# Performance work log

Hardware: AMD Instinct MI355X
Metric: run time of the kernel (lower is better)

The kernel has to match this reference:

```python
import jax, jax.numpy as jnp
import numpy as np

E = 1024      # embedding_size
K = 64        # key_size
D = 64        # head_size
S = 1024      # context_size
V = 32000     # vocab_size
H = 16        # layer_size (heads per layer)
L = 8         # num_layers
B = 2


def _pe():
    pos = jnp.arange(S, dtype=jnp.float32)[:, None]
    i = jnp.arange(E, dtype=jnp.float32)[None, :]
    ang = pos / jnp.power(10000.0, 2.0 * i / E)
    return jnp.where((jnp.arange(E) % 2 == 0)[None, :], jnp.sin(ang), jnp.cos(ang))


def setup_inputs() -> dict:
    key = jax.random.key(0)
    ks = iter(jax.random.split(key, 32))
    s = 0.02
    n = lambda shape: jax.random.normal(next(ks), shape, dtype=jnp.float32) * s
    inp = {
        "tokens": jax.random.randint(next(ks), (B, S), 0, V),
        "emb": n((V, E)),
        "pe": _pe(),
        "k1w": n((L, H, K, E)), "k1b": n((L, H, K)),
        "k2w": n((L, H, K, K)), "k2b": n((L, H, K)),
        "q1w": n((L, H, K, E)), "q1b": n((L, H, K)),
        "q2w": n((L, H, K, K)), "q2b": n((L, H, K)),
        "vw": n((L, H, D, E)), "vb": n((L, H, D)),
        "lnw": jnp.ones((L, E), jnp.float32), "lnb": jnp.zeros((L, E), jnp.float32),
        "p1w": n((L, E, E)), "p1b": n((L, E)),
        "p2w": n((L, E, E)), "p2b": n((L, E)),
        "predw": n((V, E)), "predb": n((V,)),
    }
    return inp


def reference(tokens, emb, pe, k1w, k1b, k2w, k2b, q1w, q1b, q2w, q2b,
              vw, vb, lnw, lnb, p1w, p1b, p2w, p2b, predw, predb):
    relu = jax.nn.relu
    x = emb[tokens] + pe[:tokens.shape[1]]                       # [B,S,E]
    seq = tokens.shape[1]
    # Faithful to original: tril (past+diag) gets the -1e10 penalty.
    mask = jnp.tril(jnp.ones((seq, seq), x.dtype)) * -1e10
    for l in range(L):
        # two-layer ReLU MLPs for K and Q, batched over heads
        k = relu(jnp.einsum('bse,hke->bhsk', x, k1w[l]) + k1b[l][None, :, None, :])
        k = relu(jnp.einsum('bhsk,hjk->bhsj', k, k2w[l]) + k2b[l][None, :, None, :])
        q = relu(jnp.einsum('bse,hke->bhsk', x, q1w[l]) + q1b[l][None, :, None, :])
        q = relu(jnp.einsum('bhsk,hjk->bhsj', q, q2w[l]) + q2b[l][None, :, None, :])
        v = jnp.einsum('bse,hde->bhsd', x, vw[l]) + vb[l][None, :, None, :]
        scores = jnp.einsum('bhsk,bhtk->bhst', q, k) / (K ** 0.5) + mask
        w = jax.nn.softmax(scores, axis=-1)
        o = jnp.einsum('bhst,bhtd->bhsd', w, v)                  # [B,H,S,D]
        o = o.transpose(0, 2, 1, 3).reshape(x.shape[0], seq, H * D)
        y = x + o
        mu = y.mean(-1, keepdims=True)
        var = ((y - mu) ** 2).mean(-1, keepdims=True)
        yn = (y - mu) / jnp.sqrt(var + 1e-5) * lnw[l] + lnb[l]
        h1 = relu(yn @ p1w[l].T + p1b[l])
        x = relu(h1 @ p2w[l].T + p2b[l])
    logits = x @ predw.T + predb                                 # [B,S,V]
    return logits
```

## Files before the change

### kernel.cpp

```cpp
#include <hip/hip_runtime.h>


typedef __attribute__((ext_vector_type(8))) short bf16x8;
typedef __attribute__((ext_vector_type(4))) float f32x4;

#define L_ 8
#define S_ 1024
#define E_ 1024
#define B_ 2
#define H_ 16
#define V_ 32000
#define M_ 2048

__device__ __forceinline__ unsigned short f2b(float f) {
  union { float f; unsigned int u; } v; v.f = f;
  unsigned int r = v.u + 0x7FFFu + ((v.u >> 16) & 1u);
  return (unsigned short)(r >> 16);
}

#define GLDS16(gptr, lptr)                                                            \
  __builtin_amdgcn_global_load_lds(                                                   \
      (const __attribute__((address_space(1))) unsigned int*)(gptr),                  \
      (__attribute__((address_space(3))) unsigned int*)(lptr), 16, 0, 0)

__global__ void cvt_all_kernel(
    const float* __restrict__ k1w, const float* __restrict__ q1w,
    const float* __restrict__ vw,  const float* __restrict__ k2w,
    const float* __restrict__ q2w, const float* __restrict__ p1w,
    const float* __restrict__ p2w, const float* __restrict__ predw,
    unsigned short* __restrict__ wcat, unsigned short* __restrict__ wk2,
    unsigned short* __restrict__ wq2,  unsigned short* __restrict__ wp1,
    unsigned short* __restrict__ wp2,  unsigned short* __restrict__ wpred) {
  size_t u = (size_t)blockIdx.x * 256 + threadIdx.x;
  const float* src; unsigned short* dst;
  if (u < 6291456) {
    int seg = (int)(u / 2097152);
    size_t e0 = (u - (size_t)seg * 2097152) * 4;
    const float* s = (seg == 0) ? k1w : (seg == 1) ? q1w : vw;
    src = s + e0;
    int l = (int)(e0 >> 20), off = (int)(e0 & 1048575);
    dst = wcat + (size_t)l * 3145728 + (size_t)seg * 1048576 + off;
  } else if (u < 6422528) { size_t e = (u - 6291456) * 4;  src = k2w + e;   dst = wk2 + e; }
  else if (u < 6553600)   { size_t e = (u - 6422528) * 4;  src = q2w + e;   dst = wq2 + e; }
  else if (u < 8650752)   { size_t e = (u - 6553600) * 4;  src = p1w + e;   dst = wp1 + e; }
  else if (u < 10747904)  { size_t e = (u - 8650752) * 4;  src = p2w + e;   dst = wp2 + e; }
  else                    { size_t e = (u - 10747904) * 4; src = predw + e; dst = wpred + e; }
  float4 v = *(const float4*)src;
  dst[0] = f2b(v.x); dst[1] = f2b(v.y); dst[2] = f2b(v.z); dst[3] = f2b(v.w);
}

__global__ void biascat_kernel(const float* __restrict__ k1b, const float* __restrict__ q1b,
                               const float* __restrict__ vb, float* __restrict__ bcat) {
  int i = blockIdx.x * 256 + threadIdx.x;
  int l = i / 3072, j = i - l * 3072;
  float v;
  if (j < 1024)      v = k1b[l * 1024 + j];
  else if (j < 2048) v = q1b[l * 1024 + j - 1024];
  else               v = vb [l * 1024 + j - 2048];
  bcat[i] = v;
}

__global__ void embed_kernel(const int* __restrict__ tokens, const float* __restrict__ emb,
                             const float* __restrict__ pe, float* __restrict__ x32,
                             unsigned short* __restrict__ xb) {
  int row = blockIdx.x;
  int s = row & (S_ - 1);
  int e0 = threadIdx.x * 4;
  int tok = tokens[row];
  float4 ev = *(const float4*)(emb + (size_t)tok * E_ + e0);
  float4 pv = *(const float4*)(pe + (size_t)s * E_ + e0);
  float4 v; v.x = ev.x + pv.x; v.y = ev.y + pv.y; v.z = ev.z + pv.z; v.w = ev.w + pv.w;
  *(float4*)(x32 + (size_t)row * E_ + e0) = v;
  ushort4 o; o.x = f2b(v.x); o.y = f2b(v.y); o.z = f2b(v.z); o.w = f2b(v.w);
  *(ushort4*)(xb + (size_t)row * E_ + e0) = o;
}

template <int BM, int BN, int RELU, int OBF, int OF32, int VT, int K2Q2>
__global__ __launch_bounds__(256) void gemm97(
    const unsigned short* __restrict__ A, const unsigned short* __restrict__ W,
    const float* __restrict__ bias, unsigned short* __restrict__ Cb,
    float* __restrict__ Cf, unsigned short* __restrict__ vTp,
    const unsigned short* __restrict__ wk2p, const unsigned short* __restrict__ wq2p,
    const float* __restrict__ k2bp, const float* __restrict__ q2bp,
    unsigned short* __restrict__ kbufp, unsigned short* __restrict__ qbufp,
    int K, int N, int reluN) {
  constexpr int AR = BM / 64;
  constexpr int BR = BN / 64;
  constexpr int FM = BM / 32;
  constexpr int FN = BN / 32;
  __shared__ __align__(16) unsigned short sA[BM * 32];
  __shared__ __align__(16) unsigned short sB[BN * 32];
  __shared__ __align__(16) unsigned short sC[K2Q2 ? 128 * 136 : 1];
  const int tid = threadIdx.x;
  const int lane = tid & 63, wave = tid >> 6;
  const int l16 = lane & 15, lhi = lane >> 4;

  const int gx = gridDim.x, nwg = gx * gridDim.y;
  int o = blockIdx.y * gx + blockIdx.x;
  int wg = ((nwg & 7) == 0) ? ((o & 7) * (nwg >> 3) + (o >> 3)) : o;
  const int row0 = (wg % gx) * BM, col0 = (wg / gx) * BN;

  const int wm = (wave >> 1) * (BM / 2), wn = (wave & 1) * (BN / 2);

  const int srow = wave * 16 + (lane >> 2);
  const int scol = ((lane & 3) ^ ((lane >> 3) & 3)) * 8;
  const int cx = (lhi ^ ((l16 >> 1) & 3)) * 8;

  f32x4 acc[FM][FN] = {};

  for (int k0 = 0; k0 < K; k0 += 32) {
#pragma unroll
    for (int r = 0; r < AR; r++)
      GLDS16(A + (size_t)(row0 + r * 64 + srow) * K + k0 + scol,
             sA + r * 2048 + wave * 512);
#pragma unroll
    for (int r = 0; r < BR; r++)
      GLDS16(W + (size_t)(col0 + r * 64 + srow) * K + k0 + scol,
             sB + r * 2048 + wave * 512);
    __syncthreads();

    bf16x8 af[FM], bf[FN];
#pragma unroll
    for (int i = 0; i < FM; i++)
      af[i] = *(const bf16x8*)(sA + (wm + i * 16 + l16) * 32 + cx);
#pragma unroll
    for (int j = 0; j < FN; j++)
      bf[j] = *(const bf16x8*)(sB + (wn + j * 16 + l16) * 32 + cx);
#pragma unroll
    for (int i = 0; i < FM; i++)
#pragma unroll
      for (int j = 0; j < FN; j++)
        acc[i][j] = __builtin_amdgcn_mfma_f32_16x16x32_bf16(bf[j], af[i], acc[i][j], 0, 0, 0);
    __syncthreads();
  }

  if (K2Q2 && col0 < 2048) {
#pragma unroll
    for (int j = 0; j < FN; j++) {
      const int colb = wn + j * 16 + lhi * 4;
      const float4 bv = *(const float4*)(bias + col0 + colb);
#pragma unroll
      for (int i = 0; i < FM; i++) {
        const int lrow = wm + i * 16 + l16;
        ushort4 ob;
        ob.x = f2b(fmaxf(acc[i][j][0] + bv.x, 0.f));
        ob.y = f2b(fmaxf(acc[i][j][1] + bv.y, 0.f));
        ob.z = f2b(fmaxf(acc[i][j][2] + bv.z, 0.f));
        ob.w = f2b(fmaxf(acc[i][j][3] + bv.w, 0.f));
        *(ushort4*)(sC + lrow * 136 + colb) = ob;
      }
    }
    __syncthreads();
    const int which = (col0 >= 1024) ? 1 : 0;
    const int h = ((col0 & 1023) >> 6) + (wave & 1);
    const unsigned short* W2 = (which ? wq2p : wk2p) + h * 4096;
    const float* b2 = (which ? q2bp : k2bp) + h * 64;
    unsigned short* outp = (which ? qbufp : kbufp) + h * 64;
    const int r0 = (wave >> 1) * 64;
    f32x4 acc2[4][4] = {};
#pragma unroll
    for (int ks = 0; ks < 2; ks++) {
      bf16x8 bfr[4], af2[4];
#pragma unroll
      for (int j = 0; j < 4; j++)
        bfr[j] = *(const bf16x8*)(W2 + (j * 16 + l16) * 64 + ks * 32 + (lhi << 3));
#pragma unroll
      for (int i = 0; i < 4; i++)
        af2[i] = *(const bf16x8*)(sC + (r0 + i * 16 + l16) * 136 + (wave & 1) * 64 +
                                  ks * 32 + (lhi << 3));
#pragma unroll
      for (int i = 0; i < 4; i++)
#pragma unroll
        for (int j = 0; j < 4; j++)
          acc2[i][j] = __builtin_amdgcn_mfma_f32_16x16x32_bf16(bfr[j], af2[i], acc2[i][j], 0, 0, 0);
    }
#pragma unroll
    for (int j = 0; j < 4; j++) {
      const float4 bv = *(const float4*)(b2 + j * 16 + lhi * 4);
#pragma unroll
      for (int i = 0; i < 4; i++) {
        const int row = row0 + r0 + i * 16 + l16;
        ushort4 ob;
        ob.x = f2b(fmaxf(acc2[i][j][0] + bv.x, 0.f));
        ob.y = f2b(fmaxf(acc2[i][j][1] + bv.y, 0.f));
        ob.z = f2b(fmaxf(acc2[i][j][2] + bv.z, 0.f));
        ob.w = f2b(fmaxf(acc2[i][j][3] + bv.w, 0.f));
        *(ushort4*)(outp + (size_t)row * 1024 + j * 16 + lhi * 4) = ob;
      }
    }
  } else {
#pragma unroll
    for (int j = 0; j < FN; j++) {
      const int colb = col0 + wn + j * 16 + lhi * 4;
      const float4 bv = *(const float4*)(bias + colb);
      const bool dorelu = (RELU == 1) || (RELU == 2 && colb < reluN);
#pragma unroll
      for (int i = 0; i < FM; i++) {
        const int row = row0 + wm + i * 16 + l16;
        float v0 = acc[i][j][0] + bv.x, v1 = acc[i][j][1] + bv.y;
        float v2 = acc[i][j][2] + bv.z, v3 = acc[i][j][3] + bv.w;
        if (dorelu) {
          v0 = fmaxf(v0, 0.f); v1 = fmaxf(v1, 0.f);
          v2 = fmaxf(v2, 0.f); v3 = fmaxf(v3, 0.f);
        }
        if (OBF) {
          ushort4 ob; ob.x = f2b(v0); ob.y = f2b(v1); ob.z = f2b(v2); ob.w = f2b(v3);
          *(ushort4*)(Cb + (size_t)row * N + colb) = ob;
        }
        if (OF32) {
          float4 of; of.x = v0; of.y = v1; of.z = v2; of.w = v3;
          *(float4*)(Cf + (size_t)row * N + colb) = of;
        }
        if (VT) {
          if (colb - lhi * 4 >= 2048) {
            const int hd0 = colb - 2048;
            const int bq = row >> 10, s = row & 1023;
            unsigned short* vr = vTp + ((size_t)(bq << 10) + hd0) * 1024 + s;
            vr[0] = f2b(v0); vr[1024] = f2b(v1); vr[2048] = f2b(v2); vr[3072] = f2b(v3);
          }
        }
      }
    }
  }
}

__global__ __launch_bounds__(512, 1) void gemm256_8p(
    const unsigned short* __restrict__ A, const unsigned short* __restrict__ W,
    const float* __restrict__ bias, float* __restrict__ Cf) {
  constexpr int NT = 16;
  __shared__ __align__(16) unsigned short sA[2][2][8192];
  __shared__ __align__(16) unsigned short sB[2][2][8192];
  const int tid = threadIdx.x;
  const int lane = tid & 63, wave = tid >> 6;
  const int l16 = lane & 15, lhi = lane >> 4;
  const int wr = wave >> 2, wc = wave & 3;

  const int o = blockIdx.x;
  const int wg = (o & 7) * 125 + (o >> 3);
  const int row0 = (wg & 7) * 256;
  const int col0 = (wg >> 3) * 256;

  const int srow = tid >> 2;
  const int sk   = ((tid & 3) ^ ((tid >> 3) & 3)) * 8;
  const int rsw  = (l16 >> 1) & 3;

  f32x4 acc[2][4][4] = {};

  auto stageA = [&](int kt, int s) {
    const int buf = kt & 1;
    const int kg = kt * 64 + s * 32 + sk;
#pragma unroll
    for (int i = 0; i < 2; i++)
      GLDS16(A + (size_t)(row0 + i * 128 + srow) * 1024 + kg,
             &sA[buf][s][i * 4096 + wave * 512]);
  };
  auto stageB = [&](int kt, int s) {
    const int buf = kt & 1;
    const int kg = kt * 64 + s * 32 + sk;
#pragma unroll
    for (int i = 0; i < 2; i++)
      GLDS16(W + (size_t)(col0 + i * 128 + srow) * 1024 + kg,
             &sB[buf][s][i * 4096 + wave * 512]);
  };

  stageA(0, 0); stageB(0, 0); stageA(0, 1); stageB(0, 1);

  bf16x8 af[4], bf[4];
  for (int kt = 0; kt < NT; kt++) {
    const int buf = kt & 1;
    const bool more = (kt + 1 < NT);

    asm volatile("s_waitcnt vmcnt(4)" ::: "memory");
    __builtin_amdgcn_s_barrier();
    __builtin_amdgcn_sched_barrier(0);
#pragma unroll
    for (int j = 0; j < 4; j++)
      bf[j] = *(const bf16x8*)(&sB[buf][0][(wc * 64 + j * 16 + l16) * 32 + ((lhi ^ rsw) << 3)]);
#pragma unroll
    for (int i = 0; i < 4; i++)
      af[i] = *(const bf16x8*)(&sA[buf][0][(wr * 128 + i * 16 + l16) * 32 + ((lhi ^ rsw) << 3)]);
    if (more) stageA(kt + 1, 0);
    asm volatile("s_waitcnt lgkmcnt(0)" ::: "memory");
    __builtin_amdgcn_sched_barrier(0);
    __builtin_amdgcn_s_setprio(1);
#pragma unroll
    for (int i = 0; i < 4; i++)
#pragma unroll
      for (int j = 0; j < 4; j++)
        acc[0][i][j] = __builtin_amdgcn_mfma_f32_16x16x32_bf16(bf[j], af[i], acc[0][i][j], 0, 0, 0);
    __builtin_amdgcn_s_setprio(0);
    __builtin_amdgcn_s_barrier();

#pragma unroll
    for (int i = 0; i < 4; i++)
      af[i] = *(const bf16x8*)(&sA[buf][0][(wr * 128 + 64 + i * 16 + l16) * 32 + ((lhi ^ rsw) << 3)]);
    if (more) stageB(kt + 1, 0);
    asm volatile("s_waitcnt lgkmcnt(0)" ::: "memory");
    __builtin_amdgcn_sched_barrier(0);
    __builtin_amdgcn_s_setprio(1);
#pragma unroll
    for (int i = 0; i < 4; i++)
#pragma unroll
      for (int j = 0; j < 4; j++)
        acc[1][i][j] = __builtin_amdgcn_mfma_f32_16x16x32_bf16(bf[j], af[i], acc[1][i][j], 0, 0, 0);
    __builtin_amdgcn_s_setprio(0);
    __builtin_amdgcn_s_barrier();

    if (kt == NT - 1) { asm volatile("s_waitcnt vmcnt(0)" ::: "memory"); }
    else              { asm volatile("s_waitcnt vmcnt(4)" ::: "memory"); }
    __builtin_amdgcn_s_barrier();
    __builtin_amdgcn_sched_barrier(0);
#pragma unroll
    for (int j = 0; j < 4; j++)
      bf[j] = *(const bf16x8*)(&sB[buf][1][(wc * 64 + j * 16 + l16) * 32 + ((lhi ^ rsw) << 3)]);
#pragma unroll
    for (int i = 0; i < 4; i++)
      af[i] = *(const bf16x8*)(&sA[buf][1][(wr * 128 + i * 16 + l16) * 32 + ((lhi ^ rsw) << 3)]);
    if (more) stageA(kt + 1, 1);
    asm volatile("s_waitcnt lgkmcnt(0)" ::: "memory");
    __builtin_amdgcn_sched_barrier(0);
    __builtin_amdgcn_s_setprio(1);
#pragma unroll
    for (int i = 0; i < 4; i++)
#pragma unroll
      for (int j = 0; j < 4; j++)
        acc[0][i][j] = __builtin_amdgcn_mfma_f32_16x16x32_bf16(bf[j], af[i], acc[0][i][j], 0, 0, 0);
    __builtin_amdgcn_s_setprio(0);
    __builtin_amdgcn_s_barrier();

#pragma unroll
    for (int i = 0; i < 4; i++)
      af[i] = *(const bf16x8*)(&sA[buf][1][(wr * 128 + 64 + i * 16 + l16) * 32 + ((lhi ^ rsw) << 3)]);
    if (more) stageB(kt + 1, 1);
    asm volatile("s_waitcnt lgkmcnt(0)" ::: "memory");
    __builtin_amdgcn_sched_barrier(0);
    __builtin_amdgcn_s_setprio(1);
#pragma unroll
    for (int i = 0; i < 4; i++)
#pragma unroll
      for (int j = 0; j < 4; j++)
        acc[1][i][j] = __builtin_amdgcn_mfma_f32_16x16x32_bf16(bf[j], af[i], acc[1][i][j], 0, 0, 0);
    __builtin_amdgcn_s_setprio(0);
    __builtin_amdgcn_s_barrier();
  }

#pragma unroll
  for (int rh = 0; rh < 2; rh++) {
#pragma unroll
    for (int j = 0; j < 4; j++) {
      const int colb = col0 + wc * 64 + j * 16 + lhi * 4;
      const float4 bv = *(const float4*)(bias + colb);
#pragma unroll
      for (int i = 0; i < 4; i++) {
        const int row = row0 + wr * 128 + rh * 64 + i * 16 + l16;
        float4 of;
        of.x = acc[rh][i][j][0] + bv.x; of.y = acc[rh][i][j][1] + bv.y;
        of.z = acc[rh][i][j][2] + bv.z; of.w = acc[rh][i][j][3] + bv.w;
        *(float4*)(Cf + (size_t)row * V_ + colb) = of;
      }
    }
  }
}

__global__ __launch_bounds__(128) void attn_kernel(
    const unsigned short* __restrict__ qbuf,
    const unsigned short* __restrict__ kbuf,
    const unsigned short* __restrict__ vT,
    float* __restrict__ o32) {
  constexpr int LD = 72;
  __shared__ __align__(16) unsigned short sP[2 * 16 * LD];
  const int bid = blockIdx.x;
  const int bh = bid & 31, qt = bid >> 5;
  const int b = bh >> 4, h = bh & 15;
  const int tid = threadIdx.x, lane = tid & 63, w = tid >> 6;
  const int l16 = lane & 15, lhi = lane >> 4;
  const int base = b * S_;
  const int qrow = qt * 32 + w * 16 + l16;

  bf16x8 aq[2];
#pragma unroll
  for (int ks = 0; ks < 2; ks++)
    aq[ks] = *(const bf16x8*)(qbuf + (size_t)(base + qrow) * 1024 + h * 64 + ks * 32 + (lhi << 3));

  f32x4 oacc[4] = {};
  float psum[4] = {0.f, 0.f, 0.f, 0.f};
  const int srow = qt * 32 + w * 16 + (lhi << 2);
  const int t0s = (qt == 31) ? 0 : ((qt >> 1) << 6);

  unsigned short* sPw = sP + w * 16 * LD;

  bf16x8 kA[8], vA[8], kB[8], vB[8];

  auto loadKV = [&](int t0, bf16x8* kd, bf16x8* vd) {
#pragma unroll
    for (int nt = 0; nt < 4; nt++) {
#pragma unroll
      for (int ks = 0; ks < 2; ks++) {
        kd[nt * 2 + ks] = *(const bf16x8*)(kbuf + (size_t)(base + t0 + nt * 16 + l16) * 1024 +
                                           h * 64 + ks * 32 + (lhi << 3));
        vd[nt * 2 + ks] = *(const bf16x8*)(vT + (size_t)(bh * 64 + nt * 16 + l16) * 1024 +
                                           t0 + ks * 32 + (lhi << 3));
      }
    }
  };

  auto compute = [&](int t0, const bf16x8* kc, const bf16x8* vc) {
    f32x4 sacc[4] = {};
#pragma unroll
    for (int ks = 0; ks < 2; ks++)
#pragma unroll
      for (int nt = 0; nt < 4; nt++)
        sacc[nt] = __builtin_amdgcn_mfma_f32_16x16x32_bf16(aq[ks], kc[nt * 2 + ks], sacc[nt], 0, 0, 0);
#pragma unroll
    for (int nt = 0; nt < 4; nt++) {
      int tcol = t0 + nt * 16 + l16;
#pragma unroll
      for (int r = 0; r < 4; r++) {
        const int row = srow + r;
        float e;
        if (row == S_ - 1)      e = 1.f;
        else if (tcol <= row)   e = 0.f;
        else                    e = __expf(fminf(sacc[nt][r] * 0.125f, 60.f));
        psum[r] += e;
        sPw[((lhi << 2) + r) * LD + nt * 16 + l16] = f2b(e);
      }
    }
#pragma unroll
    for (int ks = 0; ks < 2; ks++) {
      bf16x8 ap = *(const bf16x8*)(sPw + l16 * LD + ks * 32 + (lhi << 3));
#pragma unroll
      for (int nt = 0; nt < 4; nt++)
        oacc[nt] = __builtin_amdgcn_mfma_f32_16x16x32_bf16(ap, vc[nt * 2 + ks], oacc[nt], 0, 0, 0);
    }
  };

  loadKV(t0s, kA, vA);
  int t0 = t0s;
  while (true) {
    if (t0 + 64 < S_) loadKV(t0 + 64, kB, vB);
    compute(t0, kA, vA);
    t0 += 64; if (t0 >= S_) break;
    if (t0 + 64 < S_) loadKV(t0 + 64, kA, vA);
    compute(t0, kB, vB);
    t0 += 64; if (t0 >= S_) break;
  }

  float lrun[4];
#pragma unroll
  for (int r = 0; r < 4; r++) {
    float rs = psum[r];
#pragma unroll
    for (int off = 1; off < 16; off <<= 1) rs += __shfl_xor(rs, off, 16);
    lrun[r] = rs;
  }
#pragma unroll
  for (int nt = 0; nt < 4; nt++) {
#pragma unroll
    for (int r = 0; r < 4; r++) {
      int row = srow + r;
      o32[(size_t)(base + row) * 1024 + h * 64 + nt * 16 + l16] = oacc[nt][r] / lrun[r];
    }
  }
}

__global__ __launch_bounds__(256) void ln_kernel(
    const float* __restrict__ x32, const float* __restrict__ o32,
    const float* __restrict__ lnw, const float* __restrict__ lnb,
    unsigned short* __restrict__ yn) {
  __shared__ float red[8];
  const int row = blockIdx.x, tid = threadIdx.x;
  const int lane = tid & 63, wave = tid >> 6;
  const int e0 = tid * 4;
  float4 xv = *(const float4*)(x32 + (size_t)row * E_ + e0);
  float4 ov = *(const float4*)(o32 + (size_t)row * E_ + e0);
  float y0 = xv.x + ov.x, y1 = xv.y + ov.y, y2 = xv.z + ov.z, y3 = xv.w + ov.w;
  float s = y0 + y1 + y2 + y3;
  float sq = y0 * y0 + y1 * y1 + y2 * y2 + y3 * y3;
#pragma unroll
  for (int off = 32; off > 0; off >>= 1) {
    s += __shfl_xor(s, off, 64);
    sq += __shfl_xor(sq, off, 64);
  }
  if (lane == 0) { red[wave * 2] = s; red[wave * 2 + 1] = sq; }
  __syncthreads();
  float ts = red[0] + red[2] + red[4] + red[6];
  float tsq = red[1] + red[3] + red[5] + red[7];
  float mu = ts * (1.f / E_);
  float var = tsq * (1.f / E_) - mu * mu;
  float rstd = rsqrtf(var + 1e-5f);
  float4 gv = *(const float4*)(lnw + e0);
  float4 bv = *(const float4*)(lnb + e0);
  ushort4 o;
  o.x = f2b((y0 - mu) * rstd * gv.x + bv.x);
  o.y = f2b((y1 - mu) * rstd * gv.y + bv.y);
  o.z = f2b((y2 - mu) * rstd * gv.z + bv.z);
  o.w = f2b((y3 - mu) * rstd * gv.w + bv.w);
  *(ushort4*)(yn + (size_t)row * E_ + e0) = o;
}

extern "C" void kernel_launch(void* const* d_in, const int* in_sizes, int n_in,
                              void* d_out, int out_size, void* d_ws, size_t ws_size,
                              hipStream_t stream) {
  const int* tokens  = (const int*)d_in[0];
  const float* emb   = (const float*)d_in[1];
  const float* pe    = (const float*)d_in[2];
  const float* k1w   = (const float*)d_in[3];
  const float* k1b   = (const float*)d_in[4];
  const float* k2w   = (const float*)d_in[5];
  const float* k2b   = (const float*)d_in[6];
  const float* q1w   = (const float*)d_in[7];
  const float* q1b   = (const float*)d_in[8];
  const float* q2w   = (const float*)d_in[9];
  const float* q2b   = (const float*)d_in[10];
  const float* vw    = (const float*)d_in[11];
  const float* vb    = (const float*)d_in[12];
  const float* lnw   = (const float*)d_in[13];
  const float* lnb   = (const float*)d_in[14];
  const float* p1w   = (const float*)d_in[15];
  const float* p1b   = (const float*)d_in[16];
  const float* p2w   = (const float*)d_in[17];
  const float* p2b   = (const float*)d_in[18];
  const float* predw = (const float*)d_in[19];
  const float* predb = (const float*)d_in[20];
  float* out = (float*)d_out;

  char* p = (char*)d_ws;
  auto alloc = [&](size_t bytes) -> char* {
    char* r = p; p += (bytes + 255) & ~(size_t)255; return r;
  };
  unsigned short* wcat  = (unsigned short*)alloc((size_t)L_ * 3072 * 1024 * 2);
  unsigned short* wk2   = (unsigned short*)alloc((size_t)L_ * H_ * 64 * 64 * 2);
  unsigned short* wq2   = (unsigned short*)alloc((size_t)L_ * H_ * 64 * 64 * 2);
  unsigned short* wp1   = (unsigned short*)alloc((size_t)L_ * 1024 * 1024 * 2);
  unsigned short* wp2   = (unsigned short*)alloc((size_t)L_ * 1024 * 1024 * 2);
  unsigned short* wpred = (unsigned short*)alloc((size_t)V_ * 1024 * 2);
  float*          bcat  = (float*)alloc((size_t)L_ * 3072 * 4);
  float*          x32   = (float*)alloc((size_t)M_ * 1024 * 4);
  unsigned short* xb    = (unsigned short*)alloc((size_t)M_ * 1024 * 2);
  unsigned short* kbuf  = (unsigned short*)alloc((size_t)M_ * 1024 * 2);
  unsigned short* qbuf  = (unsigned short*)alloc((size_t)M_ * 1024 * 2);
  unsigned short* vTb   = (unsigned short*)alloc((size_t)32 * 64 * 1024 * 2);
  float*          o32   = (float*)alloc((size_t)M_ * 1024 * 4);
  unsigned short* yn    = (unsigned short*)alloc((size_t)M_ * 1024 * 2);
  unsigned short* h1    = (unsigned short*)alloc((size_t)M_ * 1024 * 2);
  if ((size_t)(p - (char*)d_ws) > ws_size) return;

  cvt_all_kernel<<<73984, 256, 0, stream>>>(k1w, q1w, vw, k2w, q2w, p1w, p2w, predw,
                                            wcat, wk2, wq2, wp1, wp2, wpred);
  biascat_kernel<<<96, 256, 0, stream>>>(k1b, q1b, vb, bcat);

  embed_kernel<<<M_, 256, 0, stream>>>(tokens, emb, pe, x32, xb);

  for (int l = 0; l < L_; l++) {
    const unsigned short* wcat_l = wcat + (size_t)l * 3072 * 1024;
    const float* bcat_l = bcat + (size_t)l * 3072;
    const unsigned short* wk2_l = wk2 + (size_t)l * H_ * 64 * 64;
    const unsigned short* wq2_l = wq2 + (size_t)l * H_ * 64 * 64;
    const unsigned short* wp1_l = wp1 + (size_t)l * 1024 * 1024;
    const unsigned short* wp2_l = wp2 + (size_t)l * 1024 * 1024;

    gemm97<128, 128, 2, 0, 0, 1, 1><<<dim3(16, 24), 256, 0, stream>>>(
        xb, wcat_l, bcat_l, nullptr, nullptr, vTb,
        wk2_l, wq2_l, k2b + l * 1024, q2b + l * 1024, kbuf, qbuf, 1024, 3072, 2048);
    attn_kernel<<<1024, 128, 0, stream>>>(qbuf, kbuf, vTb, o32);
    ln_kernel<<<M_, 256, 0, stream>>>(x32, o32, lnw + l * 1024, lnb + l * 1024, yn);
    gemm97<64, 128, 1, 1, 0, 0, 0><<<dim3(32, 8), 256, 0, stream>>>(
        yn, wp1_l, p1b + l * 1024, h1, nullptr, nullptr,
        nullptr, nullptr, nullptr, nullptr, nullptr, nullptr, 1024, 1024, 0);
    gemm97<64, 128, 1, 1, 1, 0, 0><<<dim3(32, 8), 256, 0, stream>>>(
        h1, wp2_l, p2b + l * 1024, xb, x32, nullptr,
        nullptr, nullptr, nullptr, nullptr, nullptr, nullptr, 1024, 1024, 0);
  }

  gemm256_8p<<<1000, 512, 0, stream>>>(xb, wpred, predb, out);
}
```

Measured before the change: 1.396 ms.

## Fuse fp32-to-bf16 weight conversion into GEMM tile loads; shrink MLP tiles

Drops the separate pre-pass that converted the K1/Q1/V and P1/P2 weights to bf16. The GEMM now reads fp32 weight tiles straight into registers, packs them to bf16 and stores them to shared memory. The fused QKV GEMM picks the k1w/q1w/vw source per column segment. This removes a large standalone read-and-write pass over the weights, but the weight tiles are now read at twice the bytes, repeatedly from L2, through synchronous register loads rather than async global-to-LDS copies. The two MLP GEMMs also switch from 64x128 to 64x64 tiles, doubling the number of workgroups.

```diff
diff --git a/kernel.cpp b/kernel.cpp
--- a/kernel.cpp
+++ b/kernel.cpp
@@ -18,33 +18,29 @@
   return (unsigned short)(r >> 16);
 }
 
+__device__ __forceinline__ bf16x8 pack8(float4 lo, float4 hi) {
+  bf16x8 v;
+  v[0] = (short)f2b(lo.x); v[1] = (short)f2b(lo.y);
+  v[2] = (short)f2b(lo.z); v[3] = (short)f2b(lo.w);
+  v[4] = (short)f2b(hi.x); v[5] = (short)f2b(hi.y);
+  v[6] = (short)f2b(hi.z); v[7] = (short)f2b(hi.w);
+  return v;
+}
+
 #define GLDS16(gptr, lptr)                                                            \
   __builtin_amdgcn_global_load_lds(                                                   \
       (const __attribute__((address_space(1))) unsigned int*)(gptr),                  \
       (__attribute__((address_space(3))) unsigned int*)(lptr), 16, 0, 0)
 
-__global__ void cvt_all_kernel(
-    const float* __restrict__ k1w, const float* __restrict__ q1w,
-    const float* __restrict__ vw,  const float* __restrict__ k2w,
-    const float* __restrict__ q2w, const float* __restrict__ p1w,
-    const float* __restrict__ p2w, const float* __restrict__ predw,
-    unsigned short* __restrict__ wcat, unsigned short* __restrict__ wk2,
-    unsigned short* __restrict__ wq2,  unsigned short* __restrict__ wp1,
-    unsigned short* __restrict__ wp2,  unsigned short* __restrict__ wpred) {
+__global__ void cvt3_kernel(const float* __restrict__ k2w, const float* __restrict__ q2w,
+                            const float* __restrict__ predw,
+                            unsigned short* __restrict__ wk2, unsigned short* __restrict__ wq2,
+                            unsigned short* __restrict__ wpred) {
   size_t u = (size_t)blockIdx.x * 256 + threadIdx.x;
   const float* src; unsigned short* dst;
-  if (u < 6291456) {
-    int seg = (int)(u / 2097152);
-    size_t e0 = (u - (size_t)seg * 2097152) * 4;
-    const float* s = (seg == 0) ? k1w : (seg == 1) ? q1w : vw;
-    src = s + e0;
-    int l = (int)(e0 >> 20), off = (int)(e0 & 1048575);
-    dst = wcat + (size_t)l * 3145728 + (size_t)seg * 1048576 + off;
-  } else if (u < 6422528) { size_t e = (u - 6291456) * 4;  src = k2w + e;   dst = wk2 + e; }
-  else if (u < 6553600)   { size_t e = (u - 6422528) * 4;  src = q2w + e;   dst = wq2 + e; }
-  else if (u < 8650752)   { size_t e = (u - 6553600) * 4;  src = p1w + e;   dst = wp1 + e; }
-  else if (u < 10747904)  { size_t e = (u - 8650752) * 4;  src = p2w + e;   dst = wp2 + e; }
-  else                    { size_t e = (u - 10747904) * 4; src = predw + e; dst = wpred + e; }
+  if (u < 131072)      { size_t e = u * 4;            src = k2w + e;   dst = wk2 + e; }
+  else if (u < 262144) { size_t e = (u - 131072) * 4; src = q2w + e;   dst = wq2 + e; }
+  else                 { size_t e = (u - 262144) * 4; src = predw + e; dst = wpred + e; }
   float4 v = *(const float4*)src;
   dst[0] = f2b(v.x); dst[1] = f2b(v.y); dst[2] = f2b(v.z); dst[3] = f2b(v.w);
 }
@@ -77,7 +73,8 @@
 
 template <int BM, int BN, int RELU, int OBF, int OF32, int VT, int K2Q2>
 __global__ __launch_bounds__(256) void gemm97(
-    const unsigned short* __restrict__ A, const unsigned short* __restrict__ W,
+    const unsigned short* __restrict__ A,
+    const float* __restrict__ W0, const float* __restrict__ W1, const float* __restrict__ W2,
     const float* __restrict__ bias, unsigned short* __restrict__ Cb,
     float* __restrict__ Cf, unsigned short* __restrict__ vTp,
     const unsigned short* __restrict__ wk2p, const unsigned short* __restrict__ wq2p,
@@ -106,17 +103,27 @@
   const int scol = ((lane & 3) ^ ((lane >> 3) & 3)) * 8;
   const int cx = (lhi ^ ((l16 >> 1) & 3)) * 8;
 
+  const int seg = col0 >> 10;
+  const float* Wp = (seg == 0) ? W0 : (seg == 1) ? W1 : W2;
+  const int nb0 = col0 - (seg << 10);
+
   f32x4 acc[FM][FN] = {};
 
   for (int k0 = 0; k0 < K; k0 += 32) {
+    float4 blo[BR], bhi[BR];
+#pragma unroll
+    for (int r = 0; r < BR; r++) {
+      const float* src = Wp + (size_t)(nb0 + r * 64 + srow) * K + k0 + scol;
+      blo[r] = *(const float4*)src;
+      bhi[r] = *(const float4*)(src + 4);
+    }
 #pragma unroll
     for (int r = 0; r < AR; r++)
       GLDS16(A + (size_t)(row0 + r * 64 + srow) * K + k0 + scol,
              sA + r * 2048 + wave * 512);
 #pragma unroll
     for (int r = 0; r < BR; r++)
-      GLDS16(W + (size_t)(col0 + r * 64 + srow) * K + k0 + scol,
-             sB + r * 2048 + wave * 512);
+      *(bf16x8*)(sB + r * 2048 + wave * 512 + lane * 8) = pack8(blo[r], bhi[r]);
     __syncthreads();
 
     bf16x8 af[FM], bf[FN];
@@ -153,7 +160,7 @@
     __syncthreads();
     const int which = (col0 >= 1024) ? 1 : 0;
     const int h = ((col0 & 1023) >> 6) + (wave & 1);
-    const unsigned short* W2 = (which ? wq2p : wk2p) + h * 4096;
+    const unsigned short* W2b = (which ? wq2p : wk2p) + h * 4096;
     const float* b2 = (which ? q2bp : k2bp) + h * 64;
     unsigned short* outp = (which ? qbufp : kbufp) + h * 64;
     const int r0 = (wave >> 1) * 64;
@@ -163,7 +170,7 @@
       bf16x8 bfr[4], af2[4];
 #pragma unroll
       for (int j = 0; j < 4; j++)
-        bfr[j] = *(const bf16x8*)(W2 + (j * 16 + l16) * 64 + ks * 32 + (lhi << 3));
+        bfr[j] = *(const bf16x8*)(W2b + (j * 16 + l16) * 64 + ks * 32 + (lhi << 3));
 #pragma unroll
       for (int i = 0; i < 4; i++)
         af2[i] = *(const bf16x8*)(sC + (r0 + i * 16 + l16) * 136 + (wave & 1) * 64 +
@@ -528,11 +535,8 @@
   auto alloc = [&](size_t bytes) -> char* {
     char* r = p; p += (bytes + 255) & ~(size_t)255; return r;
   };
-  unsigned short* wcat  = (unsigned short*)alloc((size_t)L_ * 3072 * 1024 * 2);
   unsigned short* wk2   = (unsigned short*)alloc((size_t)L_ * H_ * 64 * 64 * 2);
   unsigned short* wq2   = (unsigned short*)alloc((size_t)L_ * H_ * 64 * 64 * 2);
-  unsigned short* wp1   = (unsigned short*)alloc((size_t)L_ * 1024 * 1024 * 2);
-  unsigned short* wp2   = (unsigned short*)alloc((size_t)L_ * 1024 * 1024 * 2);
   unsigned short* wpred = (unsigned short*)alloc((size_t)V_ * 1024 * 2);
   float*          bcat  = (float*)alloc((size_t)L_ * 3072 * 4);
   float*          x32   = (float*)alloc((size_t)M_ * 1024 * 4);
@@ -545,30 +549,31 @@
   unsigned short* h1    = (unsigned short*)alloc((size_t)M_ * 1024 * 2);
   if ((size_t)(p - (char*)d_ws) > ws_size) return;
 
-  cvt_all_kernel<<<73984, 256, 0, stream>>>(k1w, q1w, vw, k2w, q2w, p1w, p2w, predw,
-                                            wcat, wk2, wq2, wp1, wp2, wpred);
+  cvt3_kernel<<<33024, 256, 0, stream>>>(k2w, q2w, predw, wk2, wq2, wpred);
   biascat_kernel<<<96, 256, 0, stream>>>(k1b, q1b, vb, bcat);
 
   embed_kernel<<<M_, 256, 0, stream>>>(tokens, emb, pe, x32, xb);
 
   for (int l = 0; l < L_; l++) {
-    const unsigned short* wcat_l = wcat + (size_t)l * 3072 * 1024;
+    const float* k1w_l = k1w + (size_t)l * 1048576;
+    const float* q1w_l = q1w + (size_t)l * 1048576;
+    const float* vw_l  = vw  + (size_t)l * 1048576;
     const float* bcat_l = bcat + (size_t)l * 3072;
     const unsigned short* wk2_l = wk2 + (size_t)l * H_ * 64 * 64;
     const unsigned short* wq2_l = wq2 + (size_t)l * H_ * 64 * 64;
-    const unsigned short* wp1_l = wp1 + (size_t)l * 1024 * 1024;
-    const unsigned short* wp2_l = wp2 + (size_t)l * 1024 * 1024;
+    const float* wp1_l = p1w + (size_t)l * 1048576;
+    const float* wp2_l = p2w + (size_t)l * 1048576;
 
     gemm97<128, 128, 2, 0, 0, 1, 1><<<dim3(16, 24), 256, 0, stream>>>(
-        xb, wcat_l, bcat_l, nullptr, nullptr, vTb,
+        xb, k1w_l, q1w_l, vw_l, bcat_l, nullptr, nullptr, vTb,
         wk2_l, wq2_l, k2b + l * 1024, q2b + l * 1024, kbuf, qbuf, 1024, 3072, 2048);
     attn_kernel<<<1024, 128, 0, stream>>>(qbuf, kbuf, vTb, o32);
     ln_kernel<<<M_, 256, 0, stream>>>(x32, o32, lnw + l * 1024, lnb + l * 1024, yn);
-    gemm97<64, 128, 1, 1, 0, 0, 0><<<dim3(32, 8), 256, 0, stream>>>(
-        yn, wp1_l, p1b + l * 1024, h1, nullptr, nullptr,
+    gemm97<64, 64, 1, 1, 0, 0, 0><<<dim3(32, 16), 256, 0, stream>>>(
+        yn, wp1_l, wp1_l, wp1_l, p1b + l * 1024, h1, nullptr, nullptr,
         nullptr, nullptr, nullptr, nullptr, nullptr, nullptr, 1024, 1024, 0);
-    gemm97<64, 128, 1, 1, 1, 0, 0><<<dim3(32, 8), 256, 0, stream>>>(
-        h1, wp2_l, p2b + l * 1024, xb, x32, nullptr,
+    gemm97<64, 64, 1, 1, 1, 0, 0><<<dim3(32, 16), 256, 0, stream>>>(
+        h1, wp2_l, wp2_l, wp2_l, p2b + l * 1024, xb, x32, nullptr,
         nullptr, nullptr, nullptr, nullptr, nullptr, nullptr, 1024, 1024, 0);
   }
 
```

Result: slower. 1.521 ms (+9.0%).
